# Kernel tuning notes

Measured on AMD Instinct MI355X. Metric: run time of the kernel, lower is better.

Reference implementation:

```python
import jax, jax.numpy as jnp
import numpy as np

B, H, S, D = 4, 8, 2048, 64

def setup_inputs() -> dict:
    key = jax.random.key(0)
    k1, k2 = jax.random.split(key)
    q = jax.random.normal(k1, (B, H, S, D), dtype=jnp.float32)
    kv = jax.random.normal(k2, (B, H, S, D), dtype=jnp.float32)
    mask = jnp.zeros((1, 1, S, S), dtype=jnp.float32)
    return {"q": q, "kv": kv, "mask": mask}

def reference(q, kv, mask):
    # score = q @ kv^T / sqrt(d_k) + mask ; softmax over last dim ; @ kv
    d_k = jnp.asarray(kv.shape[-1], dtype=q.dtype)
    score = jnp.einsum('bhqd,bhkd->bhqk', q, kv) / jnp.sqrt(d_k)
    score = score + mask
    attn = jax.nn.softmax(score, axis=-1)
    out = jnp.einsum('bhqk,bhkd->bhqd', attn, kv)
    return out
```

## Files before the change

kernel.cpp:

```cpp
#include <hip/hip_runtime.h>
#include <hip/hip_bf16.h>
#include <stdint.h>


typedef __bf16 bf16;
typedef __attribute__((ext_vector_type(8))) __bf16 bf16x8;
typedef __attribute__((ext_vector_type(4))) __bf16 bf16x4;
typedef __attribute__((ext_vector_type(4))) float floatx4;

#define SLEN 2048
#define DH   64
#define BR   64
#define BC   64
#define NKT  (SLEN / BC)
#define NQT  (SLEN / BR)
#define BH_N 32
#define LOG2E 1.44269504088896341f

#define CHB_L 1088
#define IMGB_L (8 * CHB_L)
#define IMGE_G 4096
#define BUFSZ (2 * IMGB_L)

#define AS1 __attribute__((address_space(1)))
#define AS3 __attribute__((address_space(3)))

static __device__ inline void gload_lds16(const void* g, void* l) {
    __builtin_amdgcn_global_load_lds((const AS1 uint32_t*)g, (AS3 uint32_t*)l, 16, 0, 0);
}

static_assert(BH_N == NQT, "prep kernel folds bh and qt onto one grid axis");

static __device__ inline int phys_key(int l) {
    int h = l >> 5, l5 = l & 31, q = l5 >> 3, j = l5 & 7;
    return 32 * h + (j < 4 ? 4 * q + j : 16 + 4 * q + (j - 4));
}

__global__ __launch_bounds__(256) void kv_prep(
    const float* __restrict__ kv, const float* __restrict__ mask,
    bf16* __restrict__ kvK, bf16* __restrict__ kvT, int* __restrict__ flags)
{
    __shared__ bf16 Tl[64 * 72];
    __shared__ int wany[4];
    const int kt = blockIdx.x, z = blockIdx.y;
    const int t = threadIdx.x;

    float acc = 0.f;
#pragma unroll
    for (int i = 0; i < 4; ++i) {
        int f = i * 256 + t;
        int row = f >> 4, c4 = (f & 15) * 4;
        const float4 v = *(const float4*)(mask + (size_t)(z * BR + row) * SLEN + kt * BC + c4);
        acc = fmaxf(acc, fmaxf(fmaxf(fabsf(v.x), fabsf(v.y)), fmaxf(fabsf(v.z), fabsf(v.w))));
    }
    unsigned long long any = __ballot(acc != 0.f);
    if ((t & 63) == 0) wany[t >> 6] = (any != 0ull) ? 1 : 0;

    const float* src = kv + ((size_t)z * SLEN + kt * BC) * DH;
#pragma unroll
    for (int i = 0; i < 4; ++i) {
        int f = i * 256 + t;
        int key = f >> 4, d4 = (f & 15) * 4;
        float4 v = *(const float4*)(src + (size_t)key * DH + d4);
        bf16x4 b; b[0] = (bf16)v.x; b[1] = (bf16)v.y; b[2] = (bf16)v.z; b[3] = (bf16)v.w;
        *(bf16x4*)&Tl[key * 72 + d4] = b;
    }
    __syncthreads();
    if (t == 0) flags[z * NKT + kt] = wany[0] | wany[1] | wany[2] | wany[3];

    bf16* outK = kvK + ((size_t)z * NKT + kt) * IMGE_G;
#pragma unroll
    for (int i = 0; i < 2; ++i) {
        int G = i * 256 + t;
        int c = G >> 6, L = G & 63, rl = L >> 3, p = L & 7;
        int g = (p - rl) & 7, key = 8 * c + rl;
        bf16x8 w = *(const bf16x8*)&Tl[key * 72 + g * 8];
        *(bf16x8*)(outK + (size_t)G * 8) = w;
    }
    bf16* outV = kvT + ((size_t)z * NKT + kt) * IMGE_G;
#pragma unroll
    for (int i = 0; i < 2; ++i) {
        int G = i * 256 + t;
        int c = G >> 6, L = G & 63, dl = L >> 3, p = L & 7;
        int g = (p - dl) & 7, d = 8 * c + dl;
        bf16x8 w;
#pragma unroll
        for (int j = 0; j < 8; ++j)
            w[j] = Tl[phys_key(8 * g + j) * 72 + d];
        *(bf16x8*)(outV + (size_t)G * 8) = w;
    }
}

__global__ __launch_bounds__(512) void attn_fwd6(
    const float* __restrict__ q, const float* __restrict__ mask,
    const int* __restrict__ flags,
    const bf16* __restrict__ kvK, const bf16* __restrict__ kvT,
    float* __restrict__ out)
{
    __shared__ __align__(16) char smem[2 * BUFSZ];

    const int bh = blockIdx.x;
    const int qt = blockIdx.y;
    const int q0 = qt * 128;
    const int t = threadIdx.x;
    const int wave = t >> 6, lane = t & 63;
    const int ln16 = lane & 15, quad = lane >> 4;
    const int ln8 = ln16 & 7, hb = ln16 >> 3;

    const float qscale = 0.125f * LOG2E;
    bf16x8 aq[2];
    {
        const float* qrow = q + ((size_t)bh * SLEN + q0 + wave * 16 + ln16) * DH;
#pragma unroll
        for (int kc = 0; kc < 2; ++kc) {
            float4 f0 = *(const float4*)(qrow + kc * 32 + quad * 8);
            float4 f1 = *(const float4*)(qrow + kc * 32 + quad * 8 + 4);
            bf16x8 a;
            a[0] = (bf16)(f0.x * qscale); a[1] = (bf16)(f0.y * qscale);
            a[2] = (bf16)(f0.z * qscale); a[3] = (bf16)(f0.w * qscale);
            a[4] = (bf16)(f1.x * qscale); a[5] = (bf16)(f1.y * qscale);
            a[6] = (bf16)(f1.z * qscale); a[7] = (bf16)(f1.w * qscale);
            aq[kc] = a;
        }
    }

    const int fqt = qt * 2 + (wave >> 2);
    unsigned fmask;
    {
        int ld = (lane < 32) ? flags[fqt * NKT + lane] : 0;
        fmask = (unsigned)__ballot(ld != 0);
    }

    const int kbase0 = hb * CHB_L + ln8 * 128 + (((quad + ln8) & 7) << 4);
    const int kbase1 = hb * CHB_L + ln8 * 128 + (((quad + 4 + ln8) & 7) << 4);

    floatx4 o[4];
#pragma unroll
    for (int dt = 0; dt < 4; ++dt) o[dt] = (floatx4){0.f, 0.f, 0.f, 0.f};
    float m_run = -3.0e38f, l_run = 0.f;

    const bf16* kvKb = kvK + (size_t)bh * NKT * IMGE_G;
    const bf16* kvTb = kvT + (size_t)bh * NKT * IMGE_G;

    {
        char* Kd = smem;
        char* Vd = smem + IMGB_L;
        gload_lds16(kvKb + (size_t)wave * 512 + lane * 8, Kd + wave * CHB_L);
        gload_lds16(kvTb + (size_t)wave * 512 + lane * 8, Vd + wave * CHB_L);
    }

    for (int kt = 0; kt < NKT; ++kt) {
        __syncthreads();

        if (kt + 1 < NKT) {
            char* Kd = smem + ((kt + 1) & 1) * BUFSZ;
            char* Vd = Kd + IMGB_L;
            const bf16* gK = kvKb + (size_t)(kt + 1) * IMGE_G;
            const bf16* gV = kvTb + (size_t)(kt + 1) * IMGE_G;
            gload_lds16(gK + (size_t)wave * 512 + lane * 8, Kd + wave * CHB_L);
            gload_lds16(gV + (size_t)wave * 512 + lane * 8, Vd + wave * CHB_L);
        }

        const char* Kb = smem + (kt & 1) * BUFSZ;
        const char* Vb = Kb + IMGB_L;

        floatx4 s[4];
#pragma unroll
        for (int nt = 0; nt < 4; ++nt) {
            bf16x8 k0 = *(const bf16x8*)(Kb + nt * 2176 + kbase0);
            bf16x8 k1 = *(const bf16x8*)(Kb + nt * 2176 + kbase1);
            floatx4 acc = (floatx4){0.f, 0.f, 0.f, 0.f};
            acc = __builtin_amdgcn_mfma_f32_16x16x32_bf16(k0, aq[0], acc, 0, 0, 0);
            acc = __builtin_amdgcn_mfma_f32_16x16x32_bf16(k1, aq[1], acc, 0, 0, 0);
            s[nt] = acc;
        }

        if (fmask & (1u << kt)) {
            const float* mrow = mask + (size_t)(q0 + wave * 16 + ln16) * SLEN + kt * BC;
#pragma unroll
            for (int nt = 0; nt < 4; ++nt) {
                float4 mv = *(const float4*)(mrow + 16 * nt + quad * 4);
                s[nt][0] += mv.x * LOG2E; s[nt][1] += mv.y * LOG2E;
                s[nt][2] += mv.z * LOG2E; s[nt][3] += mv.w * LOG2E;
            }
        }

        float t01 = fmaxf(fmaxf(s[0][0], s[0][1]), fmaxf(s[0][2], s[0][3]));
        float t23 = fmaxf(fmaxf(s[1][0], s[1][1]), fmaxf(s[1][2], s[1][3]));
        float t45 = fmaxf(fmaxf(s[2][0], s[2][1]), fmaxf(s[2][2], s[2][3]));
        float t67 = fmaxf(fmaxf(s[3][0], s[3][1]), fmaxf(s[3][2], s[3][3]));
        float tmax = fmaxf(fmaxf(t01, t23), fmaxf(t45, t67));
        tmax = fmaxf(tmax, __shfl_xor(tmax, 16));
        tmax = fmaxf(tmax, __shfl_xor(tmax, 32));
        float mnew = fmaxf(m_run, tmax);
        unsigned long long grew = __ballot(mnew > m_run);
        float alpha = exp2f(m_run - mnew);
        m_run = mnew;

        float rs = 0.f;
        bf16x8 pf0, pf1;
#pragma unroll
        for (int r = 0; r < 4; ++r) {
            float p0 = exp2f(s[0][r] - mnew);
            float p1 = exp2f(s[1][r] - mnew);
            float p2 = exp2f(s[2][r] - mnew);
            float p3 = exp2f(s[3][r] - mnew);
            rs += (p0 + p1) + (p2 + p3);
            pf0[r] = (bf16)p0; pf0[4 + r] = (bf16)p1;
            pf1[r] = (bf16)p2; pf1[4 + r] = (bf16)p3;
        }
        rs += __shfl_xor(rs, 16);
        rs += __shfl_xor(rs, 32);

        if (grew) {
            l_run = l_run * alpha + rs;
            float a0 = __shfl(alpha, quad * 4 + 0);
            float a1 = __shfl(alpha, quad * 4 + 1);
            float a2 = __shfl(alpha, quad * 4 + 2);
            float a3 = __shfl(alpha, quad * 4 + 3);
#pragma unroll
            for (int dt = 0; dt < 4; ++dt) {
                o[dt][0] *= a0; o[dt][1] *= a1; o[dt][2] *= a2; o[dt][3] *= a3;
            }
        } else {
            l_run += rs;
        }

#pragma unroll
        for (int dt = 0; dt < 4; ++dt) {
            bf16x8 v0 = *(const bf16x8*)(Vb + dt * 2176 + kbase0);
            bf16x8 v1 = *(const bf16x8*)(Vb + dt * 2176 + kbase1);
            o[dt] = __builtin_amdgcn_mfma_f32_16x16x32_bf16(pf0, v0, o[dt], 0, 0, 0);
            o[dt] = __builtin_amdgcn_mfma_f32_16x16x32_bf16(pf1, v1, o[dt], 0, 0, 0);
        }
    }

    float l0 = __shfl(l_run, quad * 4 + 0);
    float l1 = __shfl(l_run, quad * 4 + 1);
    float l2 = __shfl(l_run, quad * 4 + 2);
    float l3 = __shfl(l_run, quad * 4 + 3);
    float i0 = 1.f / l0, i1 = 1.f / l1, i2 = 1.f / l2, i3 = 1.f / l3;
    float* ob = out + ((size_t)bh * SLEN + q0 + wave * 16) * DH;
#pragma unroll
    for (int dt = 0; dt < 4; ++dt) {
        int col = ln16 + 16 * dt;
        ob[(quad * 4 + 0) * DH + col] = o[dt][0] * i0;
        ob[(quad * 4 + 1) * DH + col] = o[dt][1] * i1;
        ob[(quad * 4 + 2) * DH + col] = o[dt][2] * i2;
        ob[(quad * 4 + 3) * DH + col] = o[dt][3] * i3;
    }
}

#define LDT 72
__global__ __launch_bounds__(256) void attn_mask_flags(
    const float* __restrict__ mask, int* __restrict__ flags)
{
    const int kt = blockIdx.x, qt = blockIdx.y;
    const int t = threadIdx.x;
    float acc = 0.f;
#pragma unroll
    for (int i = 0; i < 4; ++i) {
        int f = i * 256 + t;
        int row = f >> 4, c4 = (f & 15) * 4;
        const float4 v = *(const float4*)(mask + (size_t)(qt * BR + row) * SLEN + kt * BC + c4);
        acc = fmaxf(acc, fmaxf(fmaxf(fabsf(v.x), fabsf(v.y)), fmaxf(fabsf(v.z), fabsf(v.w))));
    }
    unsigned long long any = __ballot(acc != 0.f);
    __shared__ int wany[4];
    if ((t & 63) == 0) wany[t >> 6] = (any != 0ull) ? 1 : 0;
    __syncthreads();
    if (t == 0) flags[qt * NKT + kt] = wany[0] | wany[1] | wany[2] | wany[3];
}

__global__ __launch_bounds__(256) void attn_fwd(
    const float* __restrict__ q, const float* __restrict__ kv,
    const float* __restrict__ mask, const int* __restrict__ flags,
    float* __restrict__ out)
{
    __shared__ __align__(16) bf16 Kl[BC * LDT];
    __shared__ __align__(16) bf16 Vt[DH * LDT];
    __shared__ __align__(16) bf16 Pl[BR * LDT];

    const int qt = blockIdx.x;
    const int bh = blockIdx.y;
    const int q0 = qt * BR;
    const int t = threadIdx.x;
    const int wave = t >> 6, lane = t & 63;
    const int ln16 = lane & 15, quad = lane >> 4;

    const float qscale = 0.125f * LOG2E;
    bf16x8 aq[2];
    {
        const float* qrow = q + ((size_t)bh * SLEN + q0 + wave * 16 + ln16) * DH;
#pragma unroll
        for (int kc = 0; kc < 2; ++kc) {
            float4 f0 = *(const float4*)(qrow + kc * 32 + quad * 8);
            float4 f1 = *(const float4*)(qrow + kc * 32 + quad * 8 + 4);
            bf16x8 a;
            a[0] = (bf16)(f0.x * qscale); a[1] = (bf16)(f0.y * qscale);
            a[2] = (bf16)(f0.z * qscale); a[3] = (bf16)(f0.w * qscale);
            a[4] = (bf16)(f1.x * qscale); a[5] = (bf16)(f1.y * qscale);
            a[6] = (bf16)(f1.z * qscale); a[7] = (bf16)(f1.w * qscale);
            aq[kc] = a;
        }
    }

    floatx4 o[4];
#pragma unroll
    for (int dt = 0; dt < 4; ++dt) o[dt] = (floatx4){0.f, 0.f, 0.f, 0.f};
    float m_run[4], l_run[4];
#pragma unroll
    for (int r = 0; r < 4; ++r) { m_run[r] = -3.0e38f; l_run[r] = 0.f; }

    const float* kvb = kv + (size_t)bh * SLEN * DH;

    for (int kt = 0; kt < NKT; ++kt) {
        float4 st[4];
        const float* kvt = kvb + (size_t)kt * BC * DH;
#pragma unroll
        for (int i = 0; i < 4; ++i) {
            int f = i * 256 + t;
            st[i] = *(const float4*)(kvt + (size_t)f * 4);
        }
        __syncthreads();
#pragma unroll
        for (int i = 0; i < 4; ++i) {
            int f = i * 256 + t;
            int key = f >> 4, d4 = (f & 15) * 4;
            bf16 b0 = (bf16)st[i].x, b1 = (bf16)st[i].y, b2 = (bf16)st[i].z, b3 = (bf16)st[i].w;
            *(bf16x4*)&Kl[key * LDT + d4] = (bf16x4){b0, b1, b2, b3};
            Vt[(d4 + 0) * LDT + key] = b0;
            Vt[(d4 + 1) * LDT + key] = b1;
            Vt[(d4 + 2) * LDT + key] = b2;
            Vt[(d4 + 3) * LDT + key] = b3;
        }
        __syncthreads();

        floatx4 s[4];
#pragma unroll
        for (int nt = 0; nt < 4; ++nt) {
            s[nt] = (floatx4){0.f, 0.f, 0.f, 0.f};
#pragma unroll
            for (int kc = 0; kc < 2; ++kc) {
                bf16x8 bk = *(const bf16x8*)&Kl[(ln16 + 16 * nt) * LDT + kc * 32 + quad * 8];
                s[nt] = __builtin_amdgcn_mfma_f32_16x16x32_bf16(aq[kc], bk, s[nt], 0, 0, 0);
            }
        }

        if (!flags || flags[qt * NKT + kt]) {
            const float* mrow = mask + (size_t)(q0 + quad * 4) * SLEN + kt * BC + ln16;
#pragma unroll
            for (int r = 0; r < 4; ++r)
#pragma unroll
                for (int nt = 0; nt < 4; ++nt)
                    s[nt][r] += mrow[(size_t)r * SLEN + nt * 16] * LOG2E;
        }

#pragma unroll
        for (int r = 0; r < 4; ++r) {
            float mx = fmaxf(fmaxf(s[0][r], s[1][r]), fmaxf(s[2][r], s[3][r]));
            mx = fmaxf(mx, __shfl_xor(mx, 1));
            mx = fmaxf(mx, __shfl_xor(mx, 2));
            mx = fmaxf(mx, __shfl_xor(mx, 4));
            mx = fmaxf(mx, __shfl_xor(mx, 8));
            float mnew = fmaxf(m_run[r], mx);
            float alpha = exp2f(m_run[r] - mnew);
            m_run[r] = mnew;
            float rs = 0.f;
#pragma unroll
            for (int nt = 0; nt < 4; ++nt) {
                float p = exp2f(s[nt][r] - mnew);
                s[nt][r] = p;
                rs += p;
            }
            rs += __shfl_xor(rs, 1);
            rs += __shfl_xor(rs, 2);
            rs += __shfl_xor(rs, 4);
            rs += __shfl_xor(rs, 8);
            l_run[r] = l_run[r] * alpha + rs;
#pragma unroll
            for (int dt = 0; dt < 4; ++dt) o[dt][r] *= alpha;
        }

#pragma unroll
        for (int nt = 0; nt < 4; ++nt)
#pragma unroll
            for (int r = 0; r < 4; ++r)
                Pl[(wave * 16 + quad * 4 + r) * LDT + ln16 + 16 * nt] = (bf16)s[nt][r];

#pragma unroll
        for (int kc2 = 0; kc2 < 2; ++kc2) {
            bf16x8 pfr = *(const bf16x8*)&Pl[(wave * 16 + ln16) * LDT + kc2 * 32 + quad * 8];
#pragma unroll
            for (int dt = 0; dt < 4; ++dt) {
                bf16x8 vf = *(const bf16x8*)&Vt[(ln16 + 16 * dt) * LDT + kc2 * 32 + quad * 8];
                o[dt] = __builtin_amdgcn_mfma_f32_16x16x32_bf16(pfr, vf, o[dt], 0, 0, 0);
            }
        }
    }

#pragma unroll
    for (int r = 0; r < 4; ++r) {
        float inv = 1.0f / l_run[r];
        int qrow = q0 + wave * 16 + quad * 4 + r;
        float* orow = out + ((size_t)bh * SLEN + qrow) * DH;
#pragma unroll
        for (int dt = 0; dt < 4; ++dt)
            orow[ln16 + 16 * dt] = o[dt][r] * inv;
    }
}

extern "C" void kernel_launch(void* const* d_in, const int* in_sizes, int n_in,
                              void* d_out, int out_size, void* d_ws, size_t ws_size,
                              hipStream_t stream)
{
    const float* q    = (const float*)d_in[0];
    const float* kv   = (const float*)d_in[1];
    const float* mask = (const float*)d_in[2];
    float* out = (float*)d_out;

    const size_t kvKoff = 4096;
    const size_t kvToff = kvKoff + (size_t)BH_N * NKT * IMGE_G * 2;
    const size_t need   = kvToff + (size_t)BH_N * NKT * IMGE_G * 2;

    if (ws_size >= need) {
        int*  flags = (int*)d_ws;
        bf16* kvK   = (bf16*)((char*)d_ws + kvKoff);
        bf16* kvT   = (bf16*)((char*)d_ws + kvToff);
        kv_prep<<<dim3(NKT, BH_N), 256, 0, stream>>>(kv, mask, kvK, kvT, flags);
        attn_fwd6<<<dim3(BH_N, SLEN / 128), 512, 0, stream>>>(q, mask, flags, kvK, kvT, out);
    } else {
        int* flags = nullptr;
        if (ws_size >= (size_t)NQT * NKT * sizeof(int)) {
            flags = (int*)d_ws;
            attn_mask_flags<<<dim3(NKT, NQT), 256, 0, stream>>>(mask, flags);
        }
        attn_fwd<<<dim3(NQT, BH_N), 256, 0, stream>>>(q, kv, mask, flags, out);
    }
}
```

Baseline: 159.7 us.

## Process two key tiles per barrier with unpadded swizzled LDS layout

The main loop now consumes two 64-key K/V tiles per iteration, prefetching the next pair into a double buffer. This halves the number of __syncthreads and online-softmax rescale steps. The padded LDS chunk stride (1088) is replaced by a dense 1024 stride, and bank conflicts are avoided instead by an extra XOR-style rotation that depends on the half-block, applied in both the prep kernel and the read offsets. LDS use doubles to 64KB, which may limit occupancy, and register pressure rises from holding two score tiles.

```diff
diff --git a/kernel.cpp b/kernel.cpp
--- a/kernel.cpp
+++ b/kernel.cpp
@@ -13,14 +13,15 @@
 #define BR   64
 #define BC   64
 #define NKT  (SLEN / BC)
+#define NEP  (NKT / 2)
 #define NQT  (SLEN / BR)
 #define BH_N 32
 #define LOG2E 1.44269504088896341f
 
-#define CHB_L 1088
-#define IMGB_L (8 * CHB_L)
+#define CHB_L  1024
+#define IMGB_L 8192
 #define IMGE_G 4096
-#define BUFSZ (2 * IMGB_L)
+#define BUF2   (4 * IMGB_L)
 
 #define AS1 __attribute__((address_space(1)))
 #define AS3 __attribute__((address_space(3)))
@@ -73,7 +74,7 @@
     for (int i = 0; i < 2; ++i) {
         int G = i * 256 + t;
         int c = G >> 6, L = G & 63, rl = L >> 3, p = L & 7;
-        int g = (p - rl) & 7, key = 8 * c + rl;
+        int g = (p - rl - 4 * (c & 1)) & 7, key = 8 * c + rl;
         bf16x8 w = *(const bf16x8*)&Tl[key * 72 + g * 8];
         *(bf16x8*)(outK + (size_t)G * 8) = w;
     }
@@ -82,7 +83,7 @@
     for (int i = 0; i < 2; ++i) {
         int G = i * 256 + t;
         int c = G >> 6, L = G & 63, dl = L >> 3, p = L & 7;
-        int g = (p - dl) & 7, d = 8 * c + dl;
+        int g = (p - dl - 4 * (c & 1)) & 7, d = 8 * c + dl;
         bf16x8 w;
 #pragma unroll
         for (int j = 0; j < 8; ++j)
@@ -91,13 +92,13 @@
     }
 }
 
-__global__ __launch_bounds__(512) void attn_fwd6(
+__global__ __launch_bounds__(512) void attn_fwd8(
     const float* __restrict__ q, const float* __restrict__ mask,
     const int* __restrict__ flags,
     const bf16* __restrict__ kvK, const bf16* __restrict__ kvT,
     float* __restrict__ out)
 {
-    __shared__ __align__(16) char smem[2 * BUFSZ];
+    __shared__ __align__(16) char smem[2 * BUF2];
 
     const int bh = blockIdx.x;
     const int qt = blockIdx.y;
@@ -131,8 +132,8 @@
         fmask = (unsigned)__ballot(ld != 0);
     }
 
-    const int kbase0 = hb * CHB_L + ln8 * 128 + (((quad + ln8) & 7) << 4);
-    const int kbase1 = hb * CHB_L + ln8 * 128 + (((quad + 4 + ln8) & 7) << 4);
+    const int kbase0 = hb * CHB_L + ln8 * 128 + (((quad + ln8 + 4 * hb) & 7) << 4);
+    const int kbase1 = hb * CHB_L + ln8 * 128 + (((quad + 4 + ln8 + 4 * hb) & 7) << 4);
 
     floatx4 o[4];
 #pragma unroll
@@ -143,53 +144,80 @@
     const bf16* kvTb = kvT + (size_t)bh * NKT * IMGE_G;
 
     {
-        char* Kd = smem;
-        char* Vd = smem + IMGB_L;
-        gload_lds16(kvKb + (size_t)wave * 512 + lane * 8, Kd + wave * CHB_L);
-        gload_lds16(kvTb + (size_t)wave * 512 + lane * 8, Vd + wave * CHB_L);
-    }
-
-    for (int kt = 0; kt < NKT; ++kt) {
+        char* B0 = smem;
+        gload_lds16(kvKb + (size_t)wave * 512 + lane * 8,           B0 +             wave * CHB_L);
+        gload_lds16(kvTb + (size_t)wave * 512 + lane * 8,           B0 + IMGB_L +    wave * CHB_L);
+        gload_lds16(kvKb + IMGE_G + (size_t)wave * 512 + lane * 8,  B0 + 2*IMGB_L +  wave * CHB_L);
+        gload_lds16(kvTb + IMGE_G + (size_t)wave * 512 + lane * 8,  B0 + 3*IMGB_L +  wave * CHB_L);
+    }
+
+    for (int e = 0; e < NEP; ++e) {
         __syncthreads();
 
-        if (kt + 1 < NKT) {
-            char* Kd = smem + ((kt + 1) & 1) * BUFSZ;
-            char* Vd = Kd + IMGB_L;
-            const bf16* gK = kvKb + (size_t)(kt + 1) * IMGE_G;
-            const bf16* gV = kvTb + (size_t)(kt + 1) * IMGE_G;
-            gload_lds16(gK + (size_t)wave * 512 + lane * 8, Kd + wave * CHB_L);
-            gload_lds16(gV + (size_t)wave * 512 + lane * 8, Vd + wave * CHB_L);
-        }
-
-        const char* Kb = smem + (kt & 1) * BUFSZ;
-        const char* Vb = Kb + IMGB_L;
-
-        floatx4 s[4];
+        if (e + 1 < NEP) {
+            char* Bn = smem + ((e + 1) & 1) * BUF2;
+            const bf16* gK0 = kvKb + (size_t)(2 * e + 2) * IMGE_G;
+            const bf16* gV0 = kvTb + (size_t)(2 * e + 2) * IMGE_G;
+            gload_lds16(gK0 + (size_t)wave * 512 + lane * 8,          Bn +            wave * CHB_L);
+            gload_lds16(gV0 + (size_t)wave * 512 + lane * 8,          Bn + IMGB_L +   wave * CHB_L);
+            gload_lds16(gK0 + IMGE_G + (size_t)wave * 512 + lane * 8, Bn + 2*IMGB_L + wave * CHB_L);
+            gload_lds16(gV0 + IMGE_G + (size_t)wave * 512 + lane * 8, Bn + 3*IMGB_L + wave * CHB_L);
+        }
+
+        const char* B  = smem + (e & 1) * BUF2;
+        const char* K0 = B;
+        const char* V0 = B + IMGB_L;
+        const char* K1 = B + 2 * IMGB_L;
+        const char* V1 = B + 3 * IMGB_L;
+
+        floatx4 s0[4], s1[4];
 #pragma unroll
         for (int nt = 0; nt < 4; ++nt) {
-            bf16x8 k0 = *(const bf16x8*)(Kb + nt * 2176 + kbase0);
-            bf16x8 k1 = *(const bf16x8*)(Kb + nt * 2176 + kbase1);
+            bf16x8 a0 = *(const bf16x8*)(K0 + nt * 2048 + kbase0);
+            bf16x8 a1 = *(const bf16x8*)(K0 + nt * 2048 + kbase1);
             floatx4 acc = (floatx4){0.f, 0.f, 0.f, 0.f};
-            acc = __builtin_amdgcn_mfma_f32_16x16x32_bf16(k0, aq[0], acc, 0, 0, 0);
-            acc = __builtin_amdgcn_mfma_f32_16x16x32_bf16(k1, aq[1], acc, 0, 0, 0);
-            s[nt] = acc;
-        }
-
-        if (fmask & (1u << kt)) {
-            const float* mrow = mask + (size_t)(q0 + wave * 16 + ln16) * SLEN + kt * BC;
+            acc = __builtin_amdgcn_mfma_f32_16x16x32_bf16(a0, aq[0], acc, 0, 0, 0);
+            acc = __builtin_amdgcn_mfma_f32_16x16x32_bf16(a1, aq[1], acc, 0, 0, 0);
+            s0[nt] = acc;
+        }
+#pragma unroll
+        for (int nt = 0; nt < 4; ++nt) {
+            bf16x8 a0 = *(const bf16x8*)(K1 + nt * 2048 + kbase0);
+            bf16x8 a1 = *(const bf16x8*)(K1 + nt * 2048 + kbase1);
+            floatx4 acc = (floatx4){0.f, 0.f, 0.f, 0.f};
+            acc = __builtin_amdgcn_mfma_f32_16x16x32_bf16(a0, aq[0], acc, 0, 0, 0);
+            acc = __builtin_amdgcn_mfma_f32_16x16x32_bf16(a1, aq[1], acc, 0, 0, 0);
+            s1[nt] = acc;
+        }
+
+        if (fmask & (1u << (2 * e))) {
+            const float* mrow = mask + (size_t)(q0 + wave * 16 + ln16) * SLEN + (2 * e) * BC;
 #pragma unroll
             for (int nt = 0; nt < 4; ++nt) {
                 float4 mv = *(const float4*)(mrow + 16 * nt + quad * 4);
-                s[nt][0] += mv.x * LOG2E; s[nt][1] += mv.y * LOG2E;
-                s[nt][2] += mv.z * LOG2E; s[nt][3] += mv.w * LOG2E;
-            }
-        }
-
-        float t01 = fmaxf(fmaxf(s[0][0], s[0][1]), fmaxf(s[0][2], s[0][3]));
-        float t23 = fmaxf(fmaxf(s[1][0], s[1][1]), fmaxf(s[1][2], s[1][3]));
-        float t45 = fmaxf(fmaxf(s[2][0], s[2][1]), fmaxf(s[2][2], s[2][3]));
-        float t67 = fmaxf(fmaxf(s[3][0], s[3][1]), fmaxf(s[3][2], s[3][3]));
-        float tmax = fmaxf(fmaxf(t01, t23), fmaxf(t45, t67));
+                s0[nt][0] += mv.x * LOG2E; s0[nt][1] += mv.y * LOG2E;
+                s0[nt][2] += mv.z * LOG2E; s0[nt][3] += mv.w * LOG2E;
+            }
+        }
+        if (fmask & (1u << (2 * e + 1))) {
+            const float* mrow = mask + (size_t)(q0 + wave * 16 + ln16) * SLEN + (2 * e + 1) * BC;
+#pragma unroll
+            for (int nt = 0; nt < 4; ++nt) {
+                float4 mv = *(const float4*)(mrow + 16 * nt + quad * 4);
+                s1[nt][0] += mv.x * LOG2E; s1[nt][1] += mv.y * LOG2E;
+                s1[nt][2] += mv.z * LOG2E; s1[nt][3] += mv.w * LOG2E;
+            }
+        }
+
+        float tm0 = s0[0][0], tm1 = s1[0][0];
+#pragma unroll
+        for (int nt = 0; nt < 4; ++nt)
+#pragma unroll
+            for (int r = 0; r < 4; ++r) {
+                tm0 = fmaxf(tm0, s0[nt][r]);
+                tm1 = fmaxf(tm1, s1[nt][r]);
+            }
+        float tmax = fmaxf(tm0, tm1);
         tmax = fmaxf(tmax, __shfl_xor(tmax, 16));
         tmax = fmaxf(tmax, __shfl_xor(tmax, 32));
         float mnew = fmaxf(m_run, tmax);
@@ -198,16 +226,22 @@
         m_run = mnew;
 
         float rs = 0.f;
-        bf16x8 pf0, pf1;
+        bf16x8 pf00, pf01, pf10, pf11;
 #pragma unroll
         for (int r = 0; r < 4; ++r) {
-            float p0 = exp2f(s[0][r] - mnew);
-            float p1 = exp2f(s[1][r] - mnew);
-            float p2 = exp2f(s[2][r] - mnew);
-            float p3 = exp2f(s[3][r] - mnew);
-            rs += (p0 + p1) + (p2 + p3);
-            pf0[r] = (bf16)p0; pf0[4 + r] = (bf16)p1;
-            pf1[r] = (bf16)p2; pf1[4 + r] = (bf16)p3;
+            float a0 = exp2f(s0[0][r] - mnew);
+            float a1 = exp2f(s0[1][r] - mnew);
+            float a2 = exp2f(s0[2][r] - mnew);
+            float a3 = exp2f(s0[3][r] - mnew);
+            float b0 = exp2f(s1[0][r] - mnew);
+            float b1 = exp2f(s1[1][r] - mnew);
+            float b2 = exp2f(s1[2][r] - mnew);
+            float b3 = exp2f(s1[3][r] - mnew);
+            rs += ((a0 + a1) + (a2 + a3)) + ((b0 + b1) + (b2 + b3));
+            pf00[r] = (bf16)a0; pf00[4 + r] = (bf16)a1;
+            pf01[r] = (bf16)a2; pf01[4 + r] = (bf16)a3;
+            pf10[r] = (bf16)b0; pf10[4 + r] = (bf16)b1;
+            pf11[r] = (bf16)b2; pf11[4 + r] = (bf16)b3;
         }
         rs += __shfl_xor(rs, 16);
         rs += __shfl_xor(rs, 32);
@@ -228,10 +262,17 @@
 
 #pragma unroll
         for (int dt = 0; dt < 4; ++dt) {
-            bf16x8 v0 = *(const bf16x8*)(Vb + dt * 2176 + kbase0);
-            bf16x8 v1 = *(const bf16x8*)(Vb + dt * 2176 + kbase1);
-            o[dt] = __builtin_amdgcn_mfma_f32_16x16x32_bf16(pf0, v0, o[dt], 0, 0, 0);
-            o[dt] = __builtin_amdgcn_mfma_f32_16x16x32_bf16(pf1, v1, o[dt], 0, 0, 0);
+            bf16x8 v0 = *(const bf16x8*)(V0 + dt * 2048 + kbase0);
+            bf16x8 v1 = *(const bf16x8*)(V0 + dt * 2048 + kbase1);
+            o[dt] = __builtin_amdgcn_mfma_f32_16x16x32_bf16(pf00, v0, o[dt], 0, 0, 0);
+            o[dt] = __builtin_amdgcn_mfma_f32_16x16x32_bf16(pf01, v1, o[dt], 0, 0, 0);
+        }
+#pragma unroll
+        for (int dt = 0; dt < 4; ++dt) {
+            bf16x8 v0 = *(const bf16x8*)(V1 + dt * 2048 + kbase0);
+            bf16x8 v1 = *(const bf16x8*)(V1 + dt * 2048 + kbase1);
+            o[dt] = __builtin_amdgcn_mfma_f32_16x16x32_bf16(pf10, v0, o[dt], 0, 0, 0);
+            o[dt] = __builtin_amdgcn_mfma_f32_16x16x32_bf16(pf11, v1, o[dt], 0, 0, 0);
         }
     }
 
@@ -393,8 +434,8 @@
             bf16x8 pfr = *(const bf16x8*)&Pl[(wave * 16 + ln16) * LDT + kc2 * 32 + quad * 8];
 #pragma unroll
             for (int dt = 0; dt < 4; ++dt) {
-                bf16x8 vf = *(const bf16x8*)&Vt[(ln16 + 16 * dt) * LDT + kc2 * 32 + quad * 8];
-                o[dt] = __builtin_amdgcn_mfma_f32_16x16x32_bf16(pfr, vf, o[dt], 0, 0, 0);
+                bf16x8 vfr = *(const bf16x8*)&Vt[(ln16 + 16 * dt) * LDT + kc2 * 32 + quad * 8];
+                o[dt] = __builtin_amdgcn_mfma_f32_16x16x32_bf16(pfr, vfr, o[dt], 0, 0, 0);
             }
         }
     }
@@ -428,7 +469,7 @@
         bf16* kvK   = (bf16*)((char*)d_ws + kvKoff);
         bf16* kvT   = (bf16*)((char*)d_ws + kvToff);
         kv_prep<<<dim3(NKT, BH_N), 256, 0, stream>>>(kv, mask, kvK, kvT, flags);
-        attn_fwd6<<<dim3(BH_N, SLEN / 128), 512, 0, stream>>>(q, mask, flags, kvK, kvT, out);
+        attn_fwd8<<<dim3(BH_N, SLEN / 128), 512, 0, stream>>>(q, mask, flags, kvK, kvT, out);
     } else {
         int* flags = nullptr;
         if (ws_size >= (size_t)NQT * NKT * sizeof(int)) {
```

After: 154.8 us. 3.0% less time.
